# Kernel optimization log

Measured on AMD Instinct MI355X. Metric: run time of the kernel, lower is better.

Reference implementation:

```python
import jax, jax.numpy as jnp
import numpy as np

NUM_USERS = 200000
NUM_ITEMS = 100000
N = NUM_USERS + NUM_ITEMS
EMB_DIM = 64
NUM_LAYERS = 3
NNZ = 4000000


def setup_inputs() -> dict:
    key = jax.random.key(0)
    k1, k2, k3, k4, k5 = jax.random.split(key, 5)
    # xavier_uniform: bound = sqrt(6/(fan_in+fan_out))
    bound = float(np.sqrt(6.0 / (NUM_USERS + EMB_DIM)))
    user_emb = jax.random.uniform(k1, (NUM_USERS, EMB_DIM), jnp.float32, -bound, bound)
    bound_i = float(np.sqrt(6.0 / (NUM_ITEMS + EMB_DIM)))
    item_emb = jax.random.uniform(k2, (NUM_ITEMS, EMB_DIM), jnp.float32, -bound_i, bound_i)
    rows = jax.random.randint(k3, (NNZ,), 0, N, dtype=jnp.int32)
    cols = jax.random.randint(k4, (NNZ,), 0, N, dtype=jnp.int32)
    vals = jax.random.uniform(k5, (NNZ,), jnp.float32)
    return {"user_emb": user_emb, "item_emb": item_emb,
            "rows": rows, "cols": cols, "vals": vals}


def _spmm(rows, cols, vals, x):
    # sparse (N,N) @ dense (N,D) via gather + segment-sum scatter
    gathered = vals[:, None] * x[cols]          # [nnz, D]
    return jax.ops.segment_sum(gathered, rows, num_segments=N)


def reference(user_emb, item_emb, rows, cols, vals):
    emb = jnp.concatenate([user_emb, item_emb], axis=0)  # [N, D]
    acc = emb  # running sum fuses the layer-mean (avoids stacking all layers)
    for _ in range(NUM_LAYERS):
        emb = _spmm(rows, cols, vals, emb)
        acc = acc + emb
    final = acc / (NUM_LAYERS + 1)
    return final[:NUM_USERS], final[NUM_USERS:]
```

## Files before the change

### kernel.cpp

```cpp
#include <hip/hip_runtime.h>


#define NUSERS 200000
#define NITEMS 100000
#define NNODES 300000
#define DIM 64
#define NNZ_CNT 4000000

#define BSHIFT 10
#define BROWS  (1 << BSHIFT)
#define NB     ((NNODES + BROWS - 1) >> BSHIFT)
#define EPB    8192


__device__ __forceinline__ unsigned short f32_to_bf16(float f) {
    unsigned u = __float_as_uint(f);
    u += 0x7FFFu + ((u >> 16) & 1u);
    return (unsigned short)(u >> 16);
}
__device__ __forceinline__ float bf16_to_f32(unsigned short h) {
    return __uint_as_float(((unsigned)h) << 16);
}


__global__ void __launch_bounds__(256) k_bhist(const int* __restrict__ rows,
                                               int* __restrict__ bcnt) {
    __shared__ int hist[NB];
    int t = threadIdx.x;
    int e0 = blockIdx.x * EPB;
    for (int i = t; i < NB; i += 256) hist[i] = 0;
    __syncthreads();
    for (int k = 0; k < EPB / 256; ++k) {
        int e = e0 + k * 256 + t;
        if (e < NNZ_CNT) atomicAdd(&hist[rows[e] >> BSHIFT], 1);
    }
    __syncthreads();
    for (int i = t; i < NB; i += 256) {
        int h = hist[i];
        if (h) atomicAdd(&bcnt[i], h);
    }
}

__global__ void k_bscan(const int* __restrict__ bcnt, int* __restrict__ bbase,
                        int* __restrict__ gcur) {
    int t = threadIdx.x;
    int v = (t < NB) ? bcnt[t] : 0;
    __shared__ int lds[512];
    lds[t] = v; __syncthreads();
    for (int d = 1; d < 512; d <<= 1) {
        int cur = lds[t];
        int add = (t >= d) ? lds[t - d] : 0;
        __syncthreads();
        lds[t] = cur + add;
        __syncthreads();
    }
    if (t < NB) {
        int e = lds[t] - v;
        bbase[t] = e;
        gcur[t]  = e;
    }
    if (t == 511) bbase[NB] = lds[511];
}


__global__ void __launch_bounds__(256) k_bucketA(
        const int* __restrict__ rows, const int* __restrict__ cols,
        const float* __restrict__ vals, int* __restrict__ gcursor,
        int2* __restrict__ staged) {
    __shared__ int hist[NB];
    __shared__ int lbase[NB];
    __shared__ int lcur[NB];
    int t = threadIdx.x;
    int e0 = blockIdx.x * EPB;
    for (int i = t; i < NB; i += 256) { hist[i] = 0; lcur[i] = 0; }
    __syncthreads();
    for (int k = 0; k < EPB / 256; ++k) {
        int e = e0 + k * 256 + t;
        if (e < NNZ_CNT) atomicAdd(&hist[rows[e] >> BSHIFT], 1);
    }
    __syncthreads();
    for (int i = t; i < NB; i += 256) {
        int h = hist[i];
        lbase[i] = h ? atomicAdd(&gcursor[i], h) : 0;
    }
    __syncthreads();
    for (int k = 0; k < EPB / 256; ++k) {
        int e = e0 + k * 256 + t;
        if (e >= NNZ_CNT) continue;
        int r = rows[e];
        int b = r >> BSHIFT;
        int p = lbase[b] + atomicAdd(&lcur[b], 1);
        int2 rec;
        rec.x = ((r & (BROWS - 1)) << 19) | cols[e];
        rec.y = __float_as_int(vals[e]);
        staged[p] = rec;
    }
}


__global__ void __launch_bounds__(1024) k_bucketB(
        const int* __restrict__ bbase, const int2* __restrict__ staged,
        int2* __restrict__ packed, int* __restrict__ rowptr) {
    __shared__ int rcnt[BROWS];
    __shared__ int cur[BROWS];
    int b = blockIdx.x;
    int t = threadIdx.x;
    int r0 = b << BSHIFT;
    int r1 = min(r0 + BROWS, NNODES);
    int nrows = r1 - r0;
    rcnt[t] = 0;
    __syncthreads();
    int start = bbase[b];
    int end   = bbase[b + 1];
    const int* sx = (const int*)staged;
    for (int idx = start + t; idx < end; idx += 1024)
        atomicAdd(&rcnt[((unsigned)sx[idx << 1]) >> 19], 1);
    __syncthreads();
    int v = rcnt[t];
    for (int d = 1; d < 1024; d <<= 1) {
        int c = rcnt[t];
        int a = (t >= d) ? rcnt[t - d] : 0;
        __syncthreads();
        rcnt[t] = c + a;
        __syncthreads();
    }
    int excl = rcnt[t] - v;
    cur[t] = start + excl;
    if (t < nrows) rowptr[r0 + t] = start + excl;
    if (b == NB - 1 && t == 0) rowptr[NNODES] = end;
    __syncthreads();
    for (int idx = start + t; idx < end; idx += 1024) {
        int2 rec = staged[idx];
        int rel = ((unsigned)rec.x) >> 19;
        int col = rec.x & 0x7FFFF;
        int pos = atomicAdd(&cur[rel], 1);
        int2 out; out.x = col; out.y = rec.y;
        packed[pos] = out;
    }
}


__global__ void k_init0(const float* __restrict__ ue, const float* __restrict__ ie,
                        unsigned short* __restrict__ xb0, float* __restrict__ acc) {
    int i = blockIdx.x * blockDim.x + threadIdx.x;
    const int total = NNODES * DIM / 4;
    if (i >= total) return;
    const int userEnd = NUSERS * DIM / 4;
    float4 v = (i < userEnd) ? ((const float4*)ue)[i]
                             : ((const float4*)ie)[i - userEnd];
    ((float4*)acc)[i] = v;
    ushort4 h;
    h.x = f32_to_bf16(v.x); h.y = f32_to_bf16(v.y);
    h.z = f32_to_bf16(v.z); h.w = f32_to_bf16(v.w);
    ((ushort4*)xb0)[i] = h;
}


template <int FINAL>
__global__ void __launch_bounds__(256) k_spmm_csr(
                           const int* __restrict__ rowptr, const int2* __restrict__ packed,
                           const unsigned short* __restrict__ xin,
                           unsigned short* __restrict__ y, float* __restrict__ acc) {
    int row  = blockIdx.x * (blockDim.x >> 6) + (threadIdx.x >> 6);
    int lane = threadIdx.x & 63;
    if (row >= NNODES) return;
    int start = __builtin_amdgcn_readfirstlane(rowptr[row]);
    int end   = __builtin_amdgcn_readfirstlane(rowptr[row + 1]);
    const unsigned short* __restrict__ xl = xin + lane;
    float s[8];
    #pragma unroll
    for (int j = 0; j < 8; ++j) s[j] = 0.f;

    if (start < end) {
        int2 e[8];
        #pragma unroll
        for (int j = 0; j < 8; ++j) {
            int k = start + j;
            e[j] = packed[(k < end) ? k : start];
        }
        for (int base = start; base < end; base += 8) {
            int nb = base + 8;
            int2 en[8];
            #pragma unroll
            for (int j = 0; j < 8; ++j) {
                int k = nb + j;
                en[j] = packed[(k < end) ? k : start];
            }
            #pragma unroll
            for (int j = 0; j < 8; ++j) {
                bool m = (base + j) < end;
                float g = bf16_to_f32(xl[(size_t)e[j].x << 6]);
                float v = m ? __int_as_float(e[j].y) : 0.0f;
                s[j] += v * g;
            }
            #pragma unroll
            for (int j = 0; j < 8; ++j) e[j] = en[j];
        }
    }
    float t0 = (s[0] + s[1]) + (s[2] + s[3]);
    float t1 = (s[4] + s[5]) + (s[6] + s[7]);
    float ssum = t0 + t1;
    size_t o = ((size_t)row << 6) + lane;
    if (FINAL) {
        acc[o] = (acc[o] + ssum) * 0.25f;
    } else {
        y[o] = f32_to_bf16(ssum);
        acc[o] += ssum;
    }
}


extern "C" void kernel_launch(void* const* d_in, const int* in_sizes, int n_in,
                              void* d_out, int out_size, void* d_ws, size_t ws_size,
                              hipStream_t stream) {
    const float* ue   = (const float*)d_in[0];
    const float* ie   = (const float*)d_in[1];
    const int*   rows = (const int*)d_in[2];
    const int*   cols = (const int*)d_in[3];
    const float* vals = (const float*)d_in[4];
    float* acc = (float*)d_out;

    const size_t embN = (size_t)NNODES * DIM;
    char* p = (char*)d_ws;
    unsigned short* xb0 = (unsigned short*)p;  p += embN * 2;
    unsigned short* xb1 = (unsigned short*)p;  p += embN * 2;
    unsigned short* xb2 = (unsigned short*)p;  p += embN * 2;
    int*   rowptr = (int*)p;              p += (size_t)(NNODES + 16) * 4;
    int*   bcnt   = (int*)p;              p += 512 * 4;
    int*   bbase  = (int*)p;              p += 512 * 4;
    int*   gcur   = (int*)p;              p += 512 * 4;
    int2*  staged = (int2*)p;             p += (size_t)NNZ_CNT * 8;
    int2*  packed = (int2*)p;             p += (size_t)NNZ_CNT * 8;

    const int row_blocks  = (NNODES + 3) / 4;
    const int edge_hblocks = (NNZ_CNT + EPB - 1) / EPB;
    const int vec_blocks = (NNODES * DIM / 4 + 255) / 256;

    hipMemsetAsync(bcnt, 0, 512 * 4, stream);
    k_bhist<<<edge_hblocks, 256, 0, stream>>>(rows, bcnt);
    k_bscan<<<1, 512, 0, stream>>>(bcnt, bbase, gcur);

    k_bucketA<<<edge_hblocks, 256, 0, stream>>>(rows, cols, vals, gcur, staged);
    k_bucketB<<<NB, 1024, 0, stream>>>(bbase, staged, packed, rowptr);

    k_init0<<<vec_blocks, 256, 0, stream>>>(ue, ie, xb0, acc);

    k_spmm_csr<0><<<row_blocks, 256, 0, stream>>>(rowptr, packed, xb0, xb1, acc);
    k_spmm_csr<0><<<row_blocks, 256, 0, stream>>>(rowptr, packed, xb1, xb2, acc);
    k_spmm_csr<1><<<row_blocks, 256, 0, stream>>>(rowptr, packed, xb2, (unsigned short*)nullptr, acc);
}
```

Baseline: 816.6 us.

## Drop fp32 accumulator traffic and simplify SpMM inner loop

The fp32 running accumulator is no longer read and written in every layer. The final layer rebuilds the mean from the original fp32 embeddings plus the bf16 layer-1 and layer-2 outputs, which removes per-layer fp32 acc read-modify-write traffic. The SpMM inner loop also drops the 8-way software-prefetch pipeline in favour of a simpler 4-way unroll with a scalar tail. Summing bf16-rounded intermediate layers instead of fp32 values slightly changes numerics, and the simpler loop may hide less load latency.

```diff
diff --git a/kernel.cpp b/kernel.cpp
--- a/kernel.cpp
+++ b/kernel.cpp
@@ -141,14 +141,13 @@
 
 
 __global__ void k_init0(const float* __restrict__ ue, const float* __restrict__ ie,
-                        unsigned short* __restrict__ xb0, float* __restrict__ acc) {
+                        unsigned short* __restrict__ xb0) {
     int i = blockIdx.x * blockDim.x + threadIdx.x;
     const int total = NNODES * DIM / 4;
     if (i >= total) return;
     const int userEnd = NUSERS * DIM / 4;
     float4 v = (i < userEnd) ? ((const float4*)ue)[i]
                              : ((const float4*)ie)[i - userEnd];
-    ((float4*)acc)[i] = v;
     ushort4 h;
     h.x = f32_to_bf16(v.x); h.y = f32_to_bf16(v.y);
     h.z = f32_to_bf16(v.z); h.w = f32_to_bf16(v.w);
@@ -157,55 +156,48 @@
 
 
 template <int FINAL>
-__global__ void __launch_bounds__(256) k_spmm_csr(
-                           const int* __restrict__ rowptr, const int2* __restrict__ packed,
-                           const unsigned short* __restrict__ xin,
-                           unsigned short* __restrict__ y, float* __restrict__ acc) {
+__global__ void __launch_bounds__(256) k_spmm(
+        const int* __restrict__ rowptr, const int2* __restrict__ packed,
+        const unsigned short* __restrict__ xin,
+        unsigned short* __restrict__ y,
+        const unsigned short* __restrict__ xprev,
+        const float* __restrict__ ue, const float* __restrict__ ie,
+        float* __restrict__ out) {
     int row  = blockIdx.x * (blockDim.x >> 6) + (threadIdx.x >> 6);
     int lane = threadIdx.x & 63;
     if (row >= NNODES) return;
     int start = __builtin_amdgcn_readfirstlane(rowptr[row]);
     int end   = __builtin_amdgcn_readfirstlane(rowptr[row + 1]);
     const unsigned short* __restrict__ xl = xin + lane;
-    float s[8];
-    #pragma unroll
-    for (int j = 0; j < 8; ++j) s[j] = 0.f;
-
-    if (start < end) {
-        int2 e[8];
-        #pragma unroll
-        for (int j = 0; j < 8; ++j) {
-            int k = start + j;
-            e[j] = packed[(k < end) ? k : start];
-        }
-        for (int base = start; base < end; base += 8) {
-            int nb = base + 8;
-            int2 en[8];
-            #pragma unroll
-            for (int j = 0; j < 8; ++j) {
-                int k = nb + j;
-                en[j] = packed[(k < end) ? k : start];
-            }
-            #pragma unroll
-            for (int j = 0; j < 8; ++j) {
-                bool m = (base + j) < end;
-                float g = bf16_to_f32(xl[(size_t)e[j].x << 6]);
-                float v = m ? __int_as_float(e[j].y) : 0.0f;
-                s[j] += v * g;
-            }
-            #pragma unroll
-            for (int j = 0; j < 8; ++j) e[j] = en[j];
-        }
-    }
-    float t0 = (s[0] + s[1]) + (s[2] + s[3]);
-    float t1 = (s[4] + s[5]) + (s[6] + s[7]);
-    float ssum = t0 + t1;
+    float s0 = 0.f, s1 = 0.f, s2 = 0.f, s3 = 0.f;
+    int idx = start;
+    for (; idx + 4 <= end; idx += 4) {
+        int2 e0 = packed[idx + 0];
+        int2 e1 = packed[idx + 1];
+        int2 e2 = packed[idx + 2];
+        int2 e3 = packed[idx + 3];
+        float g0 = bf16_to_f32(xl[(size_t)e0.x << 6]);
+        float g1 = bf16_to_f32(xl[(size_t)e1.x << 6]);
+        float g2 = bf16_to_f32(xl[(size_t)e2.x << 6]);
+        float g3 = bf16_to_f32(xl[(size_t)e3.x << 6]);
+        s0 += __int_as_float(e0.y) * g0;
+        s1 += __int_as_float(e1.y) * g1;
+        s2 += __int_as_float(e2.y) * g2;
+        s3 += __int_as_float(e3.y) * g3;
+    }
+    for (; idx < end; ++idx) {
+        int2 e = packed[idx];
+        s0 += __int_as_float(e.y) * bf16_to_f32(xl[(size_t)e.x << 6]);
+    }
+    float s = (s0 + s1) + (s2 + s3);
     size_t o = ((size_t)row << 6) + lane;
     if (FINAL) {
-        acc[o] = (acc[o] + ssum) * 0.25f;
+        float x0 = (row < NUSERS) ? ue[o] : ie[o - (size_t)NUSERS * DIM];
+        float x1 = bf16_to_f32(xprev[o]);
+        float x2 = bf16_to_f32(xin[o]);
+        out[o] = (x0 + x1 + x2 + s) * 0.25f;
     } else {
-        y[o] = f32_to_bf16(ssum);
-        acc[o] += ssum;
+        y[o] = f32_to_bf16(s);
     }
 }
 
@@ -218,7 +210,7 @@
     const int*   rows = (const int*)d_in[2];
     const int*   cols = (const int*)d_in[3];
     const float* vals = (const float*)d_in[4];
-    float* acc = (float*)d_out;
+    float* out = (float*)d_out;
 
     const size_t embN = (size_t)NNODES * DIM;
     char* p = (char*)d_ws;
@@ -243,9 +235,12 @@
     k_bucketA<<<edge_hblocks, 256, 0, stream>>>(rows, cols, vals, gcur, staged);
     k_bucketB<<<NB, 1024, 0, stream>>>(bbase, staged, packed, rowptr);
 
-    k_init0<<<vec_blocks, 256, 0, stream>>>(ue, ie, xb0, acc);
-
-    k_spmm_csr<0><<<row_blocks, 256, 0, stream>>>(rowptr, packed, xb0, xb1, acc);
-    k_spmm_csr<0><<<row_blocks, 256, 0, stream>>>(rowptr, packed, xb1, xb2, acc);
-    k_spmm_csr<1><<<row_blocks, 256, 0, stream>>>(rowptr, packed, xb2, (unsigned short*)nullptr, acc);
-}
+    k_init0<<<vec_blocks, 256, 0, stream>>>(ue, ie, xb0);
+
+    k_spmm<0><<<row_blocks, 256, 0, stream>>>(rowptr, packed, xb0, xb1,
+                                              (const unsigned short*)nullptr, ue, ie, (float*)nullptr);
+    k_spmm<0><<<row_blocks, 256, 0, stream>>>(rowptr, packed, xb1, xb2,
+                                              (const unsigned short*)nullptr, ue, ie, (float*)nullptr);
+    k_spmm<1><<<row_blocks, 256, 0, stream>>>(rowptr, packed, xb2, (unsigned short*)nullptr,
+                                              xb1, ue, ie, out);
+}
```

After: 722.6 us. 11.5% less time.
